# Optimization experiments

Measured on AMD Instinct MI355X. Metric: run time of the kernel, lower is better.

Reference implementation:

```python
import jax, jax.numpy as jnp
import numpy as np

B, S, D = 4, 2048, 1024
H = 16
DH = D // H  # 64
DFF = 4096
EPS = 1e-5


def _layer_norm(x, g, b):
    mu = jnp.mean(x, axis=-1, keepdims=True)
    var = jnp.mean((x - mu) ** 2, axis=-1, keepdims=True)
    return (x - mu) * jax.lax.rsqrt(var + EPS) * g + b


def _rope(x):
    # x: [B, S, H, DH]; same rotation for every head (module reuses one RoPE).
    inv_freq = 1.0 / (10000.0 ** (jnp.arange(0, DH, 2, dtype=jnp.float32) / DH))
    pos = jnp.arange(S, dtype=jnp.float32)
    freqs = pos[:, None] * inv_freq[None, :]            # [S, DH/2]
    cos = jnp.cos(freqs)[None, :, None, :]              # [1, S, 1, DH/2]
    sin = jnp.sin(freqs)[None, :, None, :]
    x_even = x[..., 0::2]
    x_odd = x[..., 1::2]
    r_even = x_even * cos - x_odd * sin
    r_odd = x_even * sin + x_odd * cos
    return jnp.stack([r_even, r_odd], axis=-1).reshape(x.shape)


def setup_inputs() -> dict:
    key = jax.random.key(0)
    ks = jax.random.split(key, 10)
    s_d = 1.0 / np.sqrt(D)
    s_f = 1.0 / np.sqrt(DFF)
    return {
        "x": jax.random.normal(ks[0], (B, S, D), jnp.float32),
        "Wq": jax.random.uniform(ks[1], (D, D), jnp.float32, -s_d, s_d),
        "bq": jnp.zeros((D,), jnp.float32),
        "Wk": jax.random.uniform(ks[2], (D, D), jnp.float32, -s_d, s_d),
        "bk": jnp.zeros((D,), jnp.float32),
        "Wv": jax.random.uniform(ks[3], (D, D), jnp.float32, -s_d, s_d),
        "bv": jnp.zeros((D,), jnp.float32),
        "Wo": jax.random.uniform(ks[4], (D, D), jnp.float32, -s_d, s_d),
        "bo": jnp.zeros((D,), jnp.float32),
        "W1": jax.random.uniform(ks[5], (DFF, D), jnp.float32, -s_d, s_d),
        "bf1": jnp.zeros((DFF,), jnp.float32),
        "W2": jax.random.uniform(ks[6], (D, DFF), jnp.float32, -s_f, s_f),
        "bf2": jnp.zeros((D,), jnp.float32),
        "g1": jnp.ones((D,), jnp.float32),
        "be1": jnp.zeros((D,), jnp.float32),
        "g2": jnp.ones((D,), jnp.float32),
        "be2": jnp.zeros((D,), jnp.float32),
    }


def reference(x, Wq, bq, Wk, bk, Wv, bv, Wo, bo, W1, bf1, W2, bf2, g1, be1, g2, be2):
    # Pre-LN self-attention block (dropout is identity at eval)
    residual = x
    h = _layer_norm(x, g1, be1)
    q = (h @ Wq.T + bq).reshape(B, S, H, DH)
    k = (h @ Wk.T + bk).reshape(B, S, H, DH)
    v = (h @ Wv.T + bv).reshape(B, S, H, DH)
    q = _rope(q)
    k = _rope(k)
    # scores: [B, H, Sq, Sk]
    scores = jnp.einsum("bqhd,bkhd->bhqk", q, k) / np.sqrt(DH)
    causal = jnp.tril(jnp.ones((S, S), dtype=bool))
    scores = jnp.where(causal[None, None], scores, -jnp.inf)
    attn = jax.nn.softmax(scores, axis=-1)
    out = jnp.einsum("bhqk,bkhd->bqhd", attn, v).reshape(B, S, D)
    out = out @ Wo.T + bo
    x = residual + out
    # FFN block
    residual = x
    h = _layer_norm(x, g2, be2)
    ff = jax.nn.relu(h @ W1.T + bf1) @ W2.T + bf2
    return residual + ff
```

## Files before the change

kernel.cpp:

```cpp
#include <hip/hip_runtime.h>

typedef __attribute__((ext_vector_type(8))) short bh8;
typedef __attribute__((ext_vector_type(4))) float f4;
typedef __attribute__((ext_vector_type(16))) float f16v;
typedef __attribute__((ext_vector_type(4))) unsigned int u4;

__device__ __forceinline__ unsigned short f2bf(float x) {
  unsigned int u = __float_as_uint(x);
  u += 0x7fffu + ((u >> 16) & 1u);
  return (unsigned short)(u >> 16);
}
__device__ __forceinline__ float bf2f(short x) {
  return __uint_as_float(((unsigned int)(unsigned short)x) << 16);
}
__device__ __forceinline__ unsigned cvtpk_bf16(float lo, float hi) {
  unsigned r;
  asm("v_cvt_pk_bf16_f32 %0, %1, %2" : "=v"(r) : "v"(lo), "v"(hi));
  return r;
}
__device__ __forceinline__ void gl_lds16(const short* g, short* l) {
  __builtin_amdgcn_global_load_lds(
      (const __attribute__((address_space(1))) unsigned int*)g,
      (__attribute__((address_space(3))) unsigned int*)l, 16, 0, 0);
}

#define VM4() asm volatile("s_waitcnt vmcnt(4)" ::: "memory")
#define VM0() asm volatile("s_waitcnt vmcnt(0)" ::: "memory")

__global__ __launch_bounds__(256)
void rope_table(float* __restrict__ ct, float* __restrict__ st) {
  const int idx = blockIdx.x * 256 + threadIdx.x;
  const int s = idx >> 5, j = idx & 31;
  const float invf = expf(-0.28782313662425574f * (float)j);
  const float f = (float)s * invf;
  ct[idx] = cosf(f);
  st[idx] = sinf(f);
}

__global__ __launch_bounds__(256)
void concat_bias(const float* __restrict__ bq, const float* __restrict__ bk,
                 const float* __restrict__ bv, float* __restrict__ bqkv) {
  const int i = blockIdx.x * 256 + threadIdx.x;
  bqkv[i] = (i < 1024) ? bq[i] : ((i < 2048) ? bk[i - 1024] : bv[i - 2048]);
}

__global__ __launch_bounds__(256)
void w2bf_all(const float* __restrict__ Wq, const float* __restrict__ Wk,
              const float* __restrict__ Wv, const float* __restrict__ Wo,
              const float* __restrict__ W1, const float* __restrict__ W2,
              short* __restrict__ wqkvb, short* __restrict__ wob,
              short* __restrict__ w1b, short* __restrict__ w2b) {
  const int which = blockIdx.y;
  const float* src; short* dst; int n;
  switch (which) {
    case 0: src = Wq; dst = wqkvb;                 n = 1 << 20; break;
    case 1: src = Wk; dst = wqkvb + (1 << 20);     n = 1 << 20; break;
    case 2: src = Wv; dst = wqkvb + (2 << 20);     n = 1 << 20; break;
    case 3: src = Wo; dst = wob;                   n = 1 << 20; break;
    case 4: src = W1; dst = w1b;                   n = 1 << 22; break;
    default: src = W2; dst = w2b;                  n = 1 << 22; break;
  }
  const int i = (blockIdx.x * 256 + threadIdx.x) * 4;
  if (i >= n) return;
  f4 v = *(const f4*)(src + i);
#pragma unroll
  for (int j = 0; j < 4; ++j) dst[i + j] = (short)f2bf(v[j]);
}

__global__ __launch_bounds__(256)
void layernorm_bf(const float* __restrict__ x, const float* __restrict__ g,
                  const float* __restrict__ be, short* __restrict__ out) {
  __shared__ float sb[4];
  const int row = blockIdx.x, t = threadIdx.x;
  const float* xr = x + (size_t)row * 1024;
  f4 v = *(const f4*)(xr + t * 4);
  float s = v[0] + v[1] + v[2] + v[3];
#pragma unroll
  for (int mk = 1; mk < 64; mk <<= 1) s += __shfl_xor(s, mk, 64);
  if ((t & 63) == 0) sb[t >> 6] = s;
  __syncthreads();
  const float mean = (sb[0] + sb[1] + sb[2] + sb[3]) * (1.0f / 1024.0f);
  __syncthreads();
  f4 d;
#pragma unroll
  for (int i = 0; i < 4; ++i) d[i] = v[i] - mean;
  float s2 = d[0] * d[0] + d[1] * d[1] + d[2] * d[2] + d[3] * d[3];
#pragma unroll
  for (int mk = 1; mk < 64; mk <<= 1) s2 += __shfl_xor(s2, mk, 64);
  if ((t & 63) == 0) sb[t >> 6] = s2;
  __syncthreads();
  const float var = (sb[0] + sb[1] + sb[2] + sb[3]) * (1.0f / 1024.0f);
  const float rstd = rsqrtf(var + 1e-5f);
  const f4 gg = *(const f4*)(g + t * 4);
  const f4 bb = *(const f4*)(be + t * 4);
#pragma unroll
  for (int i = 0; i < 4; ++i)
    out[(size_t)row * 1024 + t * 4 + i] = (short)f2bf(d[i] * rstd * gg[i] + bb[i]);
}

__global__ __launch_bounds__(256)
void rope_apply(short* __restrict__ qkv, const float* __restrict__ ct,
                const float* __restrict__ st) {
  const int off = blockIdx.y ? 1024 : 0;
  const int gid = blockIdx.x * 256 + threadIdx.x;
  const int row = gid >> 7, chn = gid & 127;
  const int srow = row & 2047;
  const int col = chn * 8;
  const int j0 = (col & 63) >> 1;
  short* p = qkv + (size_t)row * 3072 + off + col;
  bh8 vv = *(const bh8*)p;
  bh8 r;
#pragma unroll
  for (int pp = 0; pp < 4; ++pp) {
    const float e = bf2f(vv[2 * pp]), od = bf2f(vv[2 * pp + 1]);
    const float c = ct[srow * 32 + j0 + pp], sn = st[srow * 32 + j0 + pp];
    r[2 * pp]     = (short)f2bf(e * c - od * sn);
    r[2 * pp + 1] = (short)f2bf(e * sn + od * c);
  }
  *(bh8*)p = r;
}

__global__ __launch_bounds__(256)
void v_transpose(const short* __restrict__ qkv, short* __restrict__ vt) {
  __shared__ short tile[64][72];
  const int st = blockIdx.x, bh = blockIdx.y;
  const int b = bh >> 4, hh = bh & 15;
  const int t = threadIdx.x;
  const int r = t >> 3, c = (t & 7) * 8;
#pragma unroll
  for (int p = 0; p < 2; ++p) {
    const int s = st * 64 + p * 32 + r;
    bh8 vv = *(const bh8*)(qkv + ((size_t)b * 2048 + s) * 3072 + 2048 + hh * 64 + c);
    *(bh8*)(&tile[p * 32 + r][c]) = vv;
  }
  __syncthreads();
#pragma unroll
  for (int p = 0; p < 2; ++p) {
    const int d = p * 32 + r;
    bh8 ov;
#pragma unroll
    for (int i = 0; i < 8; ++i) ov[i] = tile[c + i][d];
    *(bh8*)(vt + ((size_t)bh * 64 + d) * 2048 + st * 64 + c) = ov;
  }
}

#define STG(dst, gbase, kt, half)                                              \
  {                                                                            \
    _Pragma("unroll") for (int cc = 0; cc < 2; ++cc) {                         \
      const int rr = (half) * 128 + cc * 64 + sr;                              \
      gl_lds16(gbase + (size_t)rr * K + (kt) * 64 + ssl * 8,                   \
               &dst[rr * 64 + (t & 7) * 8]);                                   \
    }                                                                          \
  }

#define PHASE(bf, q, STAGE_STMT, VMSTMT)                                       \
  {                                                                            \
    if ((q) == 0) {                                                            \
      _Pragma("unroll") for (int ni = 0; ni < 4; ++ni)                         \
      _Pragma("unroll") for (int kk = 0; kk < 2; ++kk)                         \
        bfrag[ni][kk] = *(const bh8*)(&Bs[bf][(wn * 64 + ni * 16 + (lane & 15)) * 64 + (((lane >> 4) + kk * 4) ^ (lane & 7)) * 8]); \
    }                                                                          \
    _Pragma("unroll") for (int j = 0; j < MFR; ++j)                            \
    _Pragma("unroll") for (int kk = 0; kk < 2; ++kk)                           \
      af[j][kk] = *(const bh8*)(&As[bf][(wm * MROWS + (MFR * (q) + j) * 16 + (lane & 15)) * 64 + (((lane >> 4) + kk * 4) ^ (lane & 7)) * 8]); \
    STAGE_STMT;                                                                \
    __builtin_amdgcn_s_barrier();                                              \
    asm volatile("s_waitcnt lgkmcnt(0)" ::: "memory");                         \
    __builtin_amdgcn_sched_barrier(0);                                         \
    __builtin_amdgcn_s_setprio(1);                                             \
    _Pragma("unroll") for (int j = 0; j < MFR; ++j)                            \
    _Pragma("unroll") for (int ni = 0; ni < 4; ++ni)                           \
    _Pragma("unroll") for (int kk = 0; kk < 2; ++kk)                           \
      acc[MFR * (q) + j][ni] = __builtin_amdgcn_mfma_f32_16x16x32_bf16(        \
          af[j][kk], bfrag[ni][kk], acc[MFR * (q) + j][ni], 0, 0, 0);          \
    __builtin_amdgcn_s_setprio(0);                                             \
    VMSTMT;                                                                    \
    __builtin_amdgcn_s_barrier();                                              \
  }

template <int BM, int RELU, int RES, int OBF16>
__global__ __launch_bounds__(512, 2)
void gemm256(const short* __restrict__ A, const short* __restrict__ Bw,
             const float* __restrict__ bias, const float* __restrict__ res,
             short* __restrict__ Cb, float* __restrict__ Cf,
             int M, int N, int K) {
  constexpr int MFR = BM / 128;
  constexpr int MROWS = BM / 2;
  __shared__ short As[2][BM * 64];
  __shared__ short Bs[2][256 * 64];
  const int t = threadIdx.x, lane = t & 63;
  const int w = t >> 6, wm = w >> 2, wn = w & 3;
  const int nwg = gridDim.x, cpx = nwg >> 3;
  int flat = blockIdx.x;
  flat = (flat & 7) * cpx + (flat >> 3);
  const int nbm = M / BM;
  const int bm = flat % nbm, bn = flat / nbm;
  const short* Ab = A + (size_t)(bm * BM) * K;
  const short* Bb = Bw + (size_t)(bn * 256) * K;
  const int nkt = K >> 6;
  const int sr = t >> 3;
  const int ssl = (t & 7) ^ (sr & 7);
  f4 acc[4 * MFR][4] = {};
  bh8 bfrag[4][2], af[MFR][2];

  STG(Bs[0], Bb, 0, 0); STG(Bs[0], Bb, 0, 1);
  if (BM == 256) { STG(As[0], Ab, 0, 0); STG(As[0], Ab, 0, 1); }
  else           { STG(As[0], Ab, 0, 0); }
  STG(Bs[1], Bb, 1, 0); STG(Bs[1], Bb, 1, 1);
  VM4();
  __builtin_amdgcn_s_barrier();

  for (int i2 = 0; i2 < nkt; i2 += 2) {
    const bool nf = (i2 + 2 < nkt);
    PHASE(0, 0, STG(As[1], Ab, i2 + 1, 0), );
    PHASE(0, 1, if (BM == 256) STG(As[1], Ab, i2 + 1, 1), );
    PHASE(0, 2, if (nf) STG(Bs[0], Bb, i2 + 2, 0), );
    PHASE(0, 3, if (nf) STG(Bs[0], Bb, i2 + 2, 1),
          if (nf) { VM4(); } else { VM0(); });
    PHASE(1, 0, if (nf) STG(As[0], Ab, i2 + 2, 0), );
    PHASE(1, 1, if (nf && BM == 256) STG(As[0], Ab, i2 + 2, 1), );
    PHASE(1, 2, if (nf) STG(Bs[1], Bb, i2 + 3, 0), );
    PHASE(1, 3, if (nf) STG(Bs[1], Bb, i2 + 3, 1), VM4());
  }

  const int rb = bm * BM + wm * MROWS + ((lane >> 4) << 2);
  const int cb = bn * 256 + wn * 64 + (lane & 15);
#pragma unroll
  for (int mi = 0; mi < 4 * MFR; ++mi) {
#pragma unroll
    for (int ni = 0; ni < 4; ++ni) {
      const int c = cb + ni * 16;
      const float bi = bias[c];
#pragma unroll
      for (int jr = 0; jr < 4; ++jr) {
        const int r = rb + mi * 16 + jr;
        float v = acc[mi][ni][jr] + bi;
        if (RES) v += res[(size_t)r * N + c];
        if (RELU) v = fmaxf(v, 0.f);
        if (OBF16) Cb[(size_t)r * N + c] = (short)f2bf(v);
        else       Cf[(size_t)r * N + c] = v;
      }
    }
  }
}

__global__ __launch_bounds__(512, 2)
void flash_attn(const short* __restrict__ qkv, const short* __restrict__ vt,
                short* __restrict__ o) {
  __shared__ short lds[2 * 2 * 64 * 72];
  const int t = threadIdx.x, lane = t & 63, w = t >> 6;
  const int l31 = lane & 31, l5 = lane >> 5;
  const int id = blockIdx.x;
  const int xcd = id & 7, y = id >> 3;
  const int bh = xcd * 8 + (y >> 2);
  const int pr = y & 3;
  const int b = bh >> 4, hh = bh & 15;
  const int r8 = t >> 3, c8 = (t & 7) * 8;
  const float NEG_INF = -__builtin_inff();

  const short* kbase = qkv + (size_t)b * 2048 * 3072 + 1024 + hh * 64;
  const short* vbase = vt + ((size_t)bh * 64 + r8) * 2048;

  for (int pass = 0; pass < 2; ++pass) {
    const int qt = pass ? pr : 7 - pr;
    const int wq0 = qt * 256 + w * 32;
    const int nt = 4 * qt + 4;

    bh8 qf[4];
    {
      const short* qrow = qkv + ((size_t)b * 2048 + wq0 + l31) * 3072 + hh * 64 + l5 * 8;
#pragma unroll
      for (int dk = 0; dk < 4; ++dk) qf[dk] = *(const bh8*)(qrow + dk * 16);
    }
    f16v o0 = {}, o1 = {};
    float mr = NEG_INF, lsum = 0.f;

    __syncthreads();
    {
      bh8 rk = *(const bh8*)(kbase + (size_t)r8 * 3072 + c8);
      bh8 rv = *(const bh8*)(vbase + c8);
      *(bh8*)(&lds[r8 * 72 + c8]) = rk;
      *(bh8*)(&lds[4608 + r8 * 72 + c8]) = rv;
    }

    for (int kt = 0; kt < nt; ++kt) {
      __syncthreads();
      const int cur = kt & 1, nxt = cur ^ 1;
      bh8 rk, rv;
      const bool more = (kt + 1 < nt);
      if (more) {
        rk = *(const bh8*)(kbase + (size_t)((kt + 1) * 64 + r8) * 3072 + c8);
        rv = *(const bh8*)(vbase + (kt + 1) * 64 + c8);
      }
      const int kvb = kt * 64;
      if (kvb <= wq0 + 31) {
        const short* Kl = &lds[cur * 9216];
        const short* Vl = &lds[cur * 9216 + 4608];
        f16v s0 = {}, s1 = {};
#pragma unroll
        for (int dk = 0; dk < 4; ++dk) {
          bh8 ka0 = *(const bh8*)(&Kl[l31 * 72 + dk * 16 + l5 * 8]);
          bh8 ka1 = *(const bh8*)(&Kl[(32 + l31) * 72 + dk * 16 + l5 * 8]);
          s0 = __builtin_amdgcn_mfma_f32_32x32x16_bf16(ka0, qf[dk], s0, 0, 0, 0);
          s1 = __builtin_amdgcn_mfma_f32_32x32x16_bf16(ka1, qf[dk], s1, 0, 0, 0);
        }
        if (kvb + 63 > wq0) {
          const int qq = wq0 + l31;
          const int kvo = kvb + l5 * 4;
#pragma unroll
          for (int r = 0; r < 16; ++r) {
            const int kv0 = kvo + (r & 3) + 8 * (r >> 2);
            if (kv0 > qq) s0[r] = NEG_INF;
            if (kv0 + 32 > qq) s1[r] = NEG_INF;
          }
        }
        float mx = s0[0];
#pragma unroll
        for (int r = 1; r < 16; ++r) mx = fmaxf(mx, s0[r]);
#pragma unroll
        for (int r = 0; r < 16; ++r) mx = fmaxf(mx, s1[r]);
        mx = fmaxf(mx, __shfl_xor(mx, 32, 64));
        const bool keep = __all(mx <= mr + 8.0f);
        float mn, al;
        if (keep) { mn = mr; al = 1.0f; }
        else {
          mn = fmaxf(mr, mx);
          al = __expf((mr - mn) * 0.125f);
          mr = mn;
        }
        float rsA = 0.f, rsB = 0.f;
#pragma unroll
        for (int r = 0; r < 16; ++r) {
          const float p0 = __expf((s0[r] - mn) * 0.125f);
          const float p1 = __expf((s1[r] - mn) * 0.125f);
          s0[r] = p0; s1[r] = p1;
          rsA += p0; rsB += p1;
        }
        float rs = rsA + rsB;
        rs += __shfl_xor(rs, 32, 64);
        if (keep) {
          lsum += rs;
        } else {
          lsum = lsum * al + rs;
#pragma unroll
          for (int r = 0; r < 16; ++r) { o0[r] *= al; o1[r] *= al; }
        }
        float pp[32];
#pragma unroll
        for (int r = 0; r < 16; ++r) { pp[r] = s0[r]; pp[16 + r] = s1[r]; }
        const bool lo32 = (l5 == 0);
#pragma unroll
        for (int ks = 0; ks < 4; ++ks) {
          const int base = (ks >> 1) * 16 + (ks & 1) * 8;
          const unsigned e0 = cvtpk_bf16(pp[base + 0], pp[base + 1]);
          const unsigned e1 = cvtpk_bf16(pp[base + 2], pp[base + 3]);
          const unsigned q0 = cvtpk_bf16(pp[base + 4], pp[base + 5]);
          const unsigned q1 = cvtpk_bf16(pp[base + 6], pp[base + 7]);
          const unsigned sel0 = lo32 ? q0 : e0;
          const unsigned sel1 = lo32 ? q1 : e1;
          const unsigned rx0 = (unsigned)__shfl_xor((int)sel0, 32, 64);
          const unsigned rx1 = (unsigned)__shfl_xor((int)sel1, 32, 64);
          u4 frag;
          frag[0] = lo32 ? e0 : rx0;
          frag[1] = lo32 ? e1 : rx1;
          frag[2] = lo32 ? rx0 : q0;
          frag[3] = lo32 ? rx1 : q1;
          const bh8 pb = *(const bh8*)&frag;
          bh8 va0 = *(const bh8*)(&Vl[l31 * 72 + ks * 16 + l5 * 8]);
          bh8 va1 = *(const bh8*)(&Vl[(32 + l31) * 72 + ks * 16 + l5 * 8]);
          o0 = __builtin_amdgcn_mfma_f32_32x32x16_bf16(va0, pb, o0, 0, 0, 0);
          o1 = __builtin_amdgcn_mfma_f32_32x32x16_bf16(va1, pb, o1, 0, 0, 0);
        }
      }
      if (more) {
        *(bh8*)(&lds[nxt * 9216 + r8 * 72 + c8]) = rk;
        *(bh8*)(&lds[nxt * 9216 + 4608 + r8 * 72 + c8]) = rv;
      }
    }

    const float inv = 1.0f / lsum;
    __syncthreads();
    short* Ot = lds;
#pragma unroll
    for (int r = 0; r < 16; ++r) {
      const int d = (r & 3) + 8 * (r >> 2) + 4 * l5;
      Ot[(w * 32 + l31) * 72 + d]      = (short)f2bf(o0[r] * inv);
      Ot[(w * 32 + l31) * 72 + 32 + d] = (short)f2bf(o1[r] * inv);
    }
    __syncthreads();
    const int qrow = t >> 1, half = t & 1;
    short* orow = o + ((size_t)b * 2048 + qt * 256 + qrow) * 1024 + hh * 64 + half * 32;
#pragma unroll
    for (int i = 0; i < 4; ++i)
      *(bh8*)(orow + i * 8) = *(const bh8*)(&Ot[qrow * 72 + half * 32 + i * 8]);
  }
}

extern "C" void kernel_launch(void* const* d_in, const int* in_sizes, int n_in,
                              void* d_out, int out_size, void* d_ws, size_t ws_size,
                              hipStream_t stream) {
  const float* x   = (const float*)d_in[0];
  const float* Wq  = (const float*)d_in[1];
  const float* bq  = (const float*)d_in[2];
  const float* Wk  = (const float*)d_in[3];
  const float* bk  = (const float*)d_in[4];
  const float* Wv  = (const float*)d_in[5];
  const float* bv  = (const float*)d_in[6];
  const float* Wo  = (const float*)d_in[7];
  const float* bo  = (const float*)d_in[8];
  const float* W1  = (const float*)d_in[9];
  const float* bf1 = (const float*)d_in[10];
  const float* W2  = (const float*)d_in[11];
  const float* bf2 = (const float*)d_in[12];
  const float* g1  = (const float*)d_in[13];
  const float* be1 = (const float*)d_in[14];
  const float* g2  = (const float*)d_in[15];
  const float* be2 = (const float*)d_in[16];
  float* out = (float*)d_out;

  char* ws = (char*)d_ws;
  const size_t MB = 1u << 20;
  short* h_ob  = (short*)ws;
  short* qkv   = (short*)(ws + 16 * MB);
  short* f1    = (short*)(ws + 16 * MB);
  short* vtb   = (short*)(ws + 64 * MB);
  short* wqkvb = (short*)(ws + 80 * MB);
  short* wob   = (short*)(ws + 86 * MB);
  short* w1b   = (short*)(ws + 88 * MB);
  short* w2b   = (short*)(ws + 96 * MB);
  float* ct    = (float*)(ws + 104 * MB);
  float* st    = ct + 65536;
  float* bqkv  = st + 65536;
  float* x2    = out;

  rope_table<<<256, 256, 0, stream>>>(ct, st);
  concat_bias<<<12, 256, 0, stream>>>(bq, bk, bv, bqkv);
  w2bf_all<<<dim3(4096, 6), 256, 0, stream>>>(Wq, Wk, Wv, Wo, W1, W2,
                                              wqkvb, wob, w1b, w2b);

  layernorm_bf<<<8192, 256, 0, stream>>>(x, g1, be1, h_ob);

  gemm256<128, 0, 0, 1><<<768, 512, 0, stream>>>(h_ob, wqkvb, bqkv, nullptr, qkv, nullptr, 8192, 3072, 1024);

  rope_apply<<<dim3(4096, 2), 256, 0, stream>>>(qkv, ct, st);

  v_transpose<<<dim3(32, 64), 256, 0, stream>>>(qkv, vtb);

  flash_attn<<<256, 512, 0, stream>>>(qkv, vtb, h_ob);

  gemm256<128, 0, 1, 0><<<256, 512, 0, stream>>>(h_ob, wob, bo, x, nullptr, x2, 8192, 1024, 1024);

  layernorm_bf<<<8192, 256, 0, stream>>>(x2, g2, be2, h_ob);

  gemm256<256, 1, 0, 1><<<512, 512, 0, stream>>>(h_ob, w1b, bf1, nullptr, f1, nullptr, 8192, 4096, 1024);

  gemm256<128, 0, 1, 0><<<256, 512, 0, stream>>>(f1, w2b, bf2, x2, nullptr, out, 8192, 1024, 4096);
}
```

Before: 397.4 us.

## Fuse V transpose into QKV GEMM epilogue and restructure BM=128 pipeline phases

```diff
diff --git a/kernel.cpp b/kernel.cpp
--- a/kernel.cpp
+++ b/kernel.cpp
@@ -1,6 +1,7 @@
 #include <hip/hip_runtime.h>
 
 typedef __attribute__((ext_vector_type(8))) short bh8;
+typedef __attribute__((ext_vector_type(4))) short sh4;
 typedef __attribute__((ext_vector_type(4))) float f4;
 typedef __attribute__((ext_vector_type(16))) float f16v;
 typedef __attribute__((ext_vector_type(4))) unsigned int u4;
@@ -120,30 +121,6 @@
   *(bh8*)p = r;
 }
 
-__global__ __launch_bounds__(256)
-void v_transpose(const short* __restrict__ qkv, short* __restrict__ vt) {
-  __shared__ short tile[64][72];
-  const int st = blockIdx.x, bh = blockIdx.y;
-  const int b = bh >> 4, hh = bh & 15;
-  const int t = threadIdx.x;
-  const int r = t >> 3, c = (t & 7) * 8;
-#pragma unroll
-  for (int p = 0; p < 2; ++p) {
-    const int s = st * 64 + p * 32 + r;
-    bh8 vv = *(const bh8*)(qkv + ((size_t)b * 2048 + s) * 3072 + 2048 + hh * 64 + c);
-    *(bh8*)(&tile[p * 32 + r][c]) = vv;
-  }
-  __syncthreads();
-#pragma unroll
-  for (int p = 0; p < 2; ++p) {
-    const int d = p * 32 + r;
-    bh8 ov;
-#pragma unroll
-    for (int i = 0; i < 8; ++i) ov[i] = tile[c + i][d];
-    *(bh8*)(vt + ((size_t)bh * 64 + d) * 2048 + st * 64 + c) = ov;
-  }
-}
-
 #define STG(dst, gbase, kt, half)                                              \
   {                                                                            \
     _Pragma("unroll") for (int cc = 0; cc < 2; ++cc) {                         \
@@ -160,28 +137,54 @@
       _Pragma("unroll") for (int kk = 0; kk < 2; ++kk)                         \
         bfrag[ni][kk] = *(const bh8*)(&Bs[bf][(wn * 64 + ni * 16 + (lane & 15)) * 64 + (((lane >> 4) + kk * 4) ^ (lane & 7)) * 8]); \
     }                                                                          \
-    _Pragma("unroll") for (int j = 0; j < MFR; ++j)                            \
+    _Pragma("unroll") for (int j = 0; j < 2; ++j)                              \
     _Pragma("unroll") for (int kk = 0; kk < 2; ++kk)                           \
-      af[j][kk] = *(const bh8*)(&As[bf][(wm * MROWS + (MFR * (q) + j) * 16 + (lane & 15)) * 64 + (((lane >> 4) + kk * 4) ^ (lane & 7)) * 8]); \
+      af[j][kk] = *(const bh8*)(&As[bf][(wm * 128 + (2 * (q) + j) * 16 + (lane & 15)) * 64 + (((lane >> 4) + kk * 4) ^ (lane & 7)) * 8]); \
     STAGE_STMT;                                                                \
     __builtin_amdgcn_s_barrier();                                              \
     asm volatile("s_waitcnt lgkmcnt(0)" ::: "memory");                         \
     __builtin_amdgcn_sched_barrier(0);                                         \
     __builtin_amdgcn_s_setprio(1);                                             \
-    _Pragma("unroll") for (int j = 0; j < MFR; ++j)                            \
+    _Pragma("unroll") for (int j = 0; j < 2; ++j)                              \
     _Pragma("unroll") for (int ni = 0; ni < 4; ++ni)                           \
     _Pragma("unroll") for (int kk = 0; kk < 2; ++kk)                           \
-      acc[MFR * (q) + j][ni] = __builtin_amdgcn_mfma_f32_16x16x32_bf16(        \
-          af[j][kk], bfrag[ni][kk], acc[MFR * (q) + j][ni], 0, 0, 0);          \
+      acc[2 * (q) + j][ni] = __builtin_amdgcn_mfma_f32_16x16x32_bf16(          \
+          af[j][kk], bfrag[ni][kk], acc[2 * (q) + j][ni], 0, 0, 0);            \
     __builtin_amdgcn_s_setprio(0);                                             \
     VMSTMT;                                                                    \
     __builtin_amdgcn_s_barrier();                                              \
   }
 
-template <int BM, int RELU, int RES, int OBF16>
+#define PH128(bf, p, STAGE_STMT, VMSTMT)                                       \
+  {                                                                            \
+    if ((p) == 0) {                                                            \
+      _Pragma("unroll") for (int ni = 0; ni < 4; ++ni)                         \
+      _Pragma("unroll") for (int kk = 0; kk < 2; ++kk)                         \
+        bfrag[ni][kk] = *(const bh8*)(&Bs[bf][(wn * 64 + ni * 16 + (lane & 15)) * 64 + (((lane >> 4) + kk * 4) ^ (lane & 7)) * 8]); \
+    }                                                                          \
+    _Pragma("unroll") for (int j = 0; j < 2; ++j)                              \
+    _Pragma("unroll") for (int kk = 0; kk < 2; ++kk)                           \
+      af[j][kk] = *(const bh8*)(&As[bf][(wm * 64 + (2 * (p) + j) * 16 + (lane & 15)) * 64 + (((lane >> 4) + kk * 4) ^ (lane & 7)) * 8]); \
+    STAGE_STMT;                                                                \
+    __builtin_amdgcn_s_barrier();                                              \
+    asm volatile("s_waitcnt lgkmcnt(0)" ::: "memory");                         \
+    __builtin_amdgcn_sched_barrier(0);                                         \
+    __builtin_amdgcn_s_setprio(1);                                             \
+    _Pragma("unroll") for (int j = 0; j < 2; ++j)                              \
+    _Pragma("unroll") for (int ni = 0; ni < 4; ++ni)                           \
+    _Pragma("unroll") for (int kk = 0; kk < 2; ++kk)                           \
+      acc[2 * (p) + j][ni] = __builtin_amdgcn_mfma_f32_16x16x32_bf16(          \
+          af[j][kk], bfrag[ni][kk], acc[2 * (p) + j][ni], 0, 0, 0);            \
+    __builtin_amdgcn_s_setprio(0);                                             \
+    VMSTMT;                                                                    \
+    __builtin_amdgcn_s_barrier();                                              \
+  }
+
+template <int BM, int RELU, int RES, int OBF16, int VOUT>
 __global__ __launch_bounds__(512, 2)
 void gemm256(const short* __restrict__ A, const short* __restrict__ Bw,
              const float* __restrict__ bias, const float* __restrict__ res,
+             short* __restrict__ Vt,
              short* __restrict__ Cb, float* __restrict__ Cf,
              int M, int N, int K) {
   constexpr int MFR = BM / 128;
@@ -201,44 +204,73 @@
   const int sr = t >> 3;
   const int ssl = (t & 7) ^ (sr & 7);
   f4 acc[4 * MFR][4] = {};
-  bh8 bfrag[4][2], af[MFR][2];
+  bh8 bfrag[4][2], af[2][2];
 
   STG(Bs[0], Bb, 0, 0); STG(Bs[0], Bb, 0, 1);
-  if (BM == 256) { STG(As[0], Ab, 0, 0); STG(As[0], Ab, 0, 1); }
-  else           { STG(As[0], Ab, 0, 0); }
+  STG(As[0], Ab, 0, 0); if (BM == 256) STG(As[0], Ab, 0, 1);
   STG(Bs[1], Bb, 1, 0); STG(Bs[1], Bb, 1, 1);
   VM4();
   __builtin_amdgcn_s_barrier();
 
-  for (int i2 = 0; i2 < nkt; i2 += 2) {
-    const bool nf = (i2 + 2 < nkt);
-    PHASE(0, 0, STG(As[1], Ab, i2 + 1, 0), );
-    PHASE(0, 1, if (BM == 256) STG(As[1], Ab, i2 + 1, 1), );
-    PHASE(0, 2, if (nf) STG(Bs[0], Bb, i2 + 2, 0), );
-    PHASE(0, 3, if (nf) STG(Bs[0], Bb, i2 + 2, 1),
-          if (nf) { VM4(); } else { VM0(); });
-    PHASE(1, 0, if (nf) STG(As[0], Ab, i2 + 2, 0), );
-    PHASE(1, 1, if (nf && BM == 256) STG(As[0], Ab, i2 + 2, 1), );
-    PHASE(1, 2, if (nf) STG(Bs[1], Bb, i2 + 3, 0), );
-    PHASE(1, 3, if (nf) STG(Bs[1], Bb, i2 + 3, 1), VM4());
+  if (BM == 256) {
+    for (int i2 = 0; i2 < nkt; i2 += 2) {
+      const bool nf = (i2 + 2 < nkt);
+      PHASE(0, 0, STG(As[1], Ab, i2 + 1, 0), );
+      PHASE(0, 1, STG(As[1], Ab, i2 + 1, 1), );
+      PHASE(0, 2, if (nf) STG(Bs[0], Bb, i2 + 2, 0), );
+      PHASE(0, 3, if (nf) STG(Bs[0], Bb, i2 + 2, 1),
+            if (nf) { VM4(); } else { VM0(); });
+      PHASE(1, 0, if (nf) STG(As[0], Ab, i2 + 2, 0), );
+      PHASE(1, 1, if (nf) STG(As[0], Ab, i2 + 2, 1), );
+      PHASE(1, 2, if (nf) STG(Bs[1], Bb, i2 + 3, 0), );
+      PHASE(1, 3, if (nf) STG(Bs[1], Bb, i2 + 3, 1), if (nf) { VM4(); });
+    }
+  } else {
+    for (int i2 = 0; i2 < nkt; i2 += 2) {
+      const bool nf = (i2 + 2 < nkt);
+      PH128(0, 0, STG(As[1], Ab, i2 + 1, 0), );
+      PH128(0, 1, if (nf) { STG(Bs[0], Bb, i2 + 2, 0); STG(Bs[0], Bb, i2 + 2, 1); },
+            if (nf) { VM4(); } else { VM0(); });
+      PH128(1, 0, if (nf) STG(As[0], Ab, i2 + 2, 0), );
+      PH128(1, 1, if (nf) { STG(Bs[1], Bb, i2 + 3, 0); STG(Bs[1], Bb, i2 + 3, 1); },
+            if (nf) { VM4(); });
+    }
   }
 
   const int rb = bm * BM + wm * MROWS + ((lane >> 4) << 2);
   const int cb = bn * 256 + wn * 64 + (lane & 15);
-#pragma unroll
-  for (int mi = 0; mi < 4 * MFR; ++mi) {
-#pragma unroll
-    for (int ni = 0; ni < 4; ++ni) {
-      const int c = cb + ni * 16;
-      const float bi = bias[c];
-#pragma unroll
-      for (int jr = 0; jr < 4; ++jr) {
-        const int r = rb + mi * 16 + jr;
-        float v = acc[mi][ni][jr] + bi;
-        if (RES) v += res[(size_t)r * N + c];
-        if (RELU) v = fmaxf(v, 0.f);
-        if (OBF16) Cb[(size_t)r * N + c] = (short)f2bf(v);
-        else       Cf[(size_t)r * N + c] = v;
+  if (VOUT && bn >= 8) {
+#pragma unroll
+    for (int mi = 0; mi < 4 * MFR; ++mi) {
+#pragma unroll
+      for (int ni = 0; ni < 4; ++ni) {
+        const int c = cb + ni * 16;
+        const float bi = bias[c];
+        const int hh = (c - 2048) >> 6, dd = (c - 2048) & 63;
+        const int r0 = rb + mi * 16;
+        const int bb2 = r0 >> 11, ss = r0 & 2047;
+        sh4 pk;
+#pragma unroll
+        for (int jr = 0; jr < 4; ++jr) pk[jr] = (short)f2bf(acc[mi][ni][jr] + bi);
+        *(sh4*)(Vt + ((size_t)(bb2 * 16 + hh) * 64 + dd) * 2048 + ss) = pk;
+      }
+    }
+  } else {
+#pragma unroll
+    for (int mi = 0; mi < 4 * MFR; ++mi) {
+#pragma unroll
+      for (int ni = 0; ni < 4; ++ni) {
+        const int c = cb + ni * 16;
+        const float bi = bias[c];
+#pragma unroll
+        for (int jr = 0; jr < 4; ++jr) {
+          const int r = rb + mi * 16 + jr;
+          float v = acc[mi][ni][jr] + bi;
+          if (RES) v += res[(size_t)r * N + c];
+          if (RELU) v = fmaxf(v, 0.f);
+          if (OBF16) Cb[(size_t)r * N + c] = (short)f2bf(v);
+          else       Cf[(size_t)r * N + c] = v;
+        }
       }
     }
   }
@@ -440,19 +472,17 @@
 
   layernorm_bf<<<8192, 256, 0, stream>>>(x, g1, be1, h_ob);
 
-  gemm256<128, 0, 0, 1><<<768, 512, 0, stream>>>(h_ob, wqkvb, bqkv, nullptr, qkv, nullptr, 8192, 3072, 1024);
+  gemm256<128, 0, 0, 1, 1><<<768, 512, 0, stream>>>(h_ob, wqkvb, bqkv, nullptr, vtb, qkv, nullptr, 8192, 3072, 1024);
 
   rope_apply<<<dim3(4096, 2), 256, 0, stream>>>(qkv, ct, st);
 
-  v_transpose<<<dim3(32, 64), 256, 0, stream>>>(qkv, vtb);
-
   flash_attn<<<256, 512, 0, stream>>>(qkv, vtb, h_ob);
 
-  gemm256<128, 0, 1, 0><<<256, 512, 0, stream>>>(h_ob, wob, bo, x, nullptr, x2, 8192, 1024, 1024);
+  gemm256<128, 0, 1, 0, 0><<<256, 512, 0, stream>>>(h_ob, wob, bo, x, nullptr, nullptr, x2, 8192, 1024, 1024);
 
   layernorm_bf<<<8192, 256, 0, stream>>>(x2, g2, be2, h_ob);
 
-  gemm256<256, 1, 0, 1><<<512, 512, 0, stream>>>(h_ob, w1b, bf1, nullptr, f1, nullptr, 8192, 4096, 1024);
-
-  gemm256<128, 0, 1, 0><<<256, 512, 0, stream>>>(f1, w2b, bf2, x2, nullptr, out, 8192, 1024, 4096);
-}
+  gemm256<256, 1, 0, 1, 0><<<512, 512, 0, stream>>>(h_ob, w1b, bf1, nullptr, nullptr, f1, nullptr, 8192, 4096, 1024);
+
+  gemm256<128, 0, 1, 0, 0><<<256, 512, 0, stream>>>(f1, w2b, bf2, x2, nullptr, nullptr, out, 8192, 1024, 4096);
+}
```

Result: no change. 402.6 us (+1.3%).
